# Kernel tuning notes

Hardware: AMD Instinct MI355X
Metric: run time of the kernel (lower is better)

## Reference

```python
import jax, jax.numpy as jnp
import numpy as np

BIN_SIZE = 128
DIST_MULT = 0.1
LN_EPS = 1e-6


def setup_inputs() -> dict:
    key = jax.random.key(0)
    ks = jax.random.split(key, 24)
    B, N, D, DD, H = 8, 25600, 256, 128, 128
    s = 0.02
    inp = {
        'x': jax.random.normal(ks[0], (B, N, D), dtype=jnp.float32),
        'msk': jax.random.randint(ks[1], (B, N), 0, 2) > 0,
        'ln_g': jnp.ones((D,), jnp.float32),
        'ln_b': jnp.zeros((D,), jnp.float32),
        # ffn_dist: Linear(256,128) ELU Linear(128,128) ELU Linear(128,128)
        'w1': s * jax.random.normal(ks[2], (D, H), jnp.float32),
        'b1': jnp.zeros((H,), jnp.float32),
        'w2': s * jax.random.normal(ks[3], (H, H), jnp.float32),
        'b2': jnp.zeros((H,), jnp.float32),
        'w3': s * jax.random.normal(ks[4], (H, DD), jnp.float32),
        'b3': jnp.zeros((DD,), jnp.float32),
        # LSH codebook random rotations [distance_dim, max_num_bins//2]
        'codebook': jax.random.normal(ks[5], (DD, 100), jnp.float32),
        # two GHConvDense layers, hidden_dim=output_dim=256
        'theta0': jax.random.normal(ks[6], (D, D), jnp.float32) * s,
        'wh0': jax.random.normal(ks[7], (D, D), jnp.float32) * s,
        'wt0': jax.random.normal(ks[8], (D, D), jnp.float32) * s,
        'bt0': jnp.zeros((D,), jnp.float32),
        'theta1': jax.random.normal(ks[9], (D, D), jnp.float32) * s,
        'wh1': jax.random.normal(ks[10], (D, D), jnp.float32) * s,
        'wt1': jax.random.normal(ks[11], (D, D), jnp.float32) * s,
        'bt1': jnp.zeros((D,), jnp.float32),
    }
    return inp


def _forward(x, msk, ln_g, ln_b, w1, b1, w2, b2, w3, b3, codebook,
             theta0, wh0, wt0, bt0, theta1, wh1, wt1, bt1):
    B, n_elems, D = x.shape
    pad = (-n_elems) % BIN_SIZE  # static python int
    if pad:
        x = jnp.pad(x, ((0, 0), (0, pad), (0, 0)))
        msk = jnp.pad(msk, ((0, 0), (0, pad)), constant_values=True)
    Np = n_elems + pad
    n_bins = Np // BIN_SIZE

    # layernorm
    mu = jnp.mean(x, -1, keepdims=True)
    var = jnp.mean(jnp.square(x - mu), -1, keepdims=True)
    xn = (x - mu) * jax.lax.rsqrt(var + LN_EPS) * ln_g + ln_b

    # distance FFN + dist activation (elu)
    h = jax.nn.elu(xn @ w1 + b1)
    h = jax.nn.elu(h @ w2 + b2)
    x_dist = jax.nn.elu(h @ w3 + b3)  # [B, Np, distance_dim]

    # LSH binning
    mul = x_dist @ codebook[:, :max(1, n_bins // 2)]
    cmul = jnp.concatenate([mul, -mul], axis=-1)  # [B, Np, n_bins]
    a = jnp.argmax(cmul, axis=-1)
    bin_idx = a + jnp.where(msk, 0, n_bins - 1)
    bins_split = jnp.argsort(bin_idx, axis=-1)  # [B, Np]

    # gather into bins
    xm = jnp.take_along_axis(x_dist, bins_split[..., None], axis=1)
    xm = xm.reshape(B, n_bins, BIN_SIZE, x_dist.shape[-1])
    xb = jnp.take_along_axis(xn, bins_split[..., None], axis=1)
    xb = xb.reshape(B, n_bins, BIN_SIZE, D)
    mskf = jnp.take_along_axis(msk, bins_split, axis=1)
    mskf = mskf.reshape(B, n_bins, BIN_SIZE, 1).astype(x.dtype)

    # pairwise Gaussian kernel within each bin
    xk = xm * mskf
    nsq = jnp.sum(jnp.square(xk), -1)  # [B, nb, P]
    inner = jnp.einsum('bnpd,bnqd->bnpq', xk, xk)
    d2 = nsq[..., :, None] - 2.0 * inner + nsq[..., None, :]
    dist = jnp.sqrt(jnp.clip(d2, 1e-6, 1e6))
    dm = jnp.clip(jnp.exp(-DIST_MULT * dist), 0.0, 1.0)
    dm = dm * mskf * jnp.swapaxes(mskf, -1, -2)  # mask rows & cols [B,nb,P,P]

    # gated graph convolutions
    for th, wh, wt, bt in ((theta0, wh0, wt0, bt0), (theta1, wh1, wt1, bt1)):
        xmk = xb * mskf
        f_hom = jnp.einsum('bnpq,bnqd->bnpd', dm, (xmk @ th) * mskf)
        f_het = xmk @ wh
        gate = jax.nn.sigmoid(xb @ wt + bt)
        xb = jax.nn.elu(gate * f_hom + (1.0 - gate) * f_het) * mskf

    # reverse LSH scatter
    xb_flat = xb.reshape(B, Np, D)
    ret = jax.vmap(lambda idx, pts: jnp.zeros((Np, D), pts.dtype).at[idx].set(pts))(
        bins_split, xb_flat)
    return ret[:, :n_elems, :]


def reference(x, msk, ln_g, ln_b, w1, b1, w2, b2, w3, b3, codebook,
              theta0, wh0, wt0, bt0, theta1, wh1, wt1, bt1):
    return _forward(x, msk, ln_g, ln_b, w1, b1, w2, b2, w3, b3, codebook,
                    theta0, wh0, wt0, bt0, theta1, wh1, wt1, bt1)
```

## Files before the change

kernel.cpp:

```cpp
#include <hip/hip_runtime.h>
#include <math.h>

#define B_ 8
#define NP_ 25600
#define T_ (B_*NP_)
#define D_ 256
#define H_ 128
#define DD_ 128
#define NBINS_ 200
#define NIDS_ 400
#define PB_ 128
#define NC_ 100
#define GT_ (B_*NBINS_)

typedef __attribute__((ext_vector_type(8))) short bf16x8;
typedef __attribute__((ext_vector_type(4))) float f32x4;
typedef __attribute__((ext_vector_type(4))) unsigned short u16x4;
typedef unsigned short u16;

__device__ __forceinline__ float eluf(float v){ return v > 0.f ? v : expm1f(v); }
__device__ __forceinline__ u16 f2bf(float f){
  union { float f; unsigned u; } v; v.f = f;
  unsigned r = v.u + 0x7fffu + ((v.u >> 16) & 1u);
  return (u16)(r >> 16);
}
__device__ __forceinline__ float bf2f(u16 h){
  union { unsigned u; float f; } v; v.u = ((unsigned)h) << 16; return v.f;
}

__device__ __forceinline__ void gl16(void* lds, const void* g){
  __builtin_amdgcn_global_load_lds((const __attribute__((address_space(1))) void*)g,
                                   (__attribute__((address_space(3))) void*)lds, 16, 0, 0);
}

__global__ void k_mask_detect(const unsigned int* __restrict__ m, int* __restrict__ flags){
  int any_f1 = 0, any_o = 0;
  for (int i = blockIdx.x*blockDim.x + threadIdx.x; i < T_/4; i += gridDim.x*blockDim.x){
    unsigned int w = m[i];
    if (w == 0x3F800000u) any_f1 = 1;
    else if (w > 1u) any_o = 1;
  }
  if (any_f1) atomicOr(&flags[0], 1);
  if (any_o)  atomicOr(&flags[1], 1);
}

__global__ void k_mask_convert(const void* __restrict__ m, const int* __restrict__ flags,
                               float* __restrict__ mskf){
  int i = blockIdx.x*256 + threadIdx.x;
  int mode = flags[0] ? 2 : (flags[1] ? 1 : 0);
  bool v;
  if (mode == 2)      v = ((const float*)m)[i] != 0.f;
  else if (mode == 1) v = ((const unsigned char*)m)[i] != 0;
  else                v = ((const int*)m)[i] != 0;
  mskf[i] = v ? 1.f : 0.f;
}

__global__ __launch_bounds__(256) void k_ln(const float* __restrict__ x,
    const float* __restrict__ g, const float* __restrict__ b, float* __restrict__ xn){
  const int wave = threadIdx.x >> 6, lane = threadIdx.x & 63;
  const long t = (long)blockIdx.x*4 + wave;
  float4 v = ((const float4*)(x + t*D_))[lane];
  float s  = v.x + v.y + v.z + v.w;
  float s2 = v.x*v.x + v.y*v.y + v.z*v.z + v.w*v.w;
  #pragma unroll
  for (int o = 32; o; o >>= 1){ s += __shfl_xor(s, o); s2 += __shfl_xor(s2, o); }
  const float mu = s * (1.f/D_);
  float var = s2*(1.f/D_) - mu*mu;
  var = fmaxf(var, 0.f);
  const float rs = rsqrtf(var + 1e-6f);
  float4 gg = ((const float4*)g)[lane];
  float4 bb = ((const float4*)b)[lane];
  float4 o4;
  o4.x = (v.x-mu)*rs*gg.x + bb.x;
  o4.y = (v.y-mu)*rs*gg.y + bb.y;
  o4.z = (v.z-mu)*rs*gg.z + bb.z;
  o4.w = (v.w-mu)*rs*gg.w + bb.w;
  ((float4*)(xn + t*D_))[lane] = o4;
}

template<int K>
__global__ __launch_bounds__(256) void k_gemm2(const float* __restrict__ A,
    const float* __restrict__ W, const float* __restrict__ bias, float* __restrict__ C){
  __shared__ __align__(16) float As[32*132];
  __shared__ __align__(16) float Bs[32*132];
  const size_t m0 = (size_t)blockIdx.x * 128;
  const int tid = threadIdx.x;
  const int tm = tid >> 4, tn = tid & 15;
  float acc[8][8] = {};
  for (int kc = 0; kc < K; kc += 32){
    __syncthreads();
    {
      const int r = tid >> 1, kq = (tid & 1) * 16;
      const float* src = &A[(m0 + r)*(size_t)K + kc + kq];
      #pragma unroll
      for (int q = 0; q < 4; ++q){
        const float4 v = ((const float4*)src)[q];
        As[(kq + q*4 + 0)*132 + r] = v.x;
        As[(kq + q*4 + 1)*132 + r] = v.y;
        As[(kq + q*4 + 2)*132 + r] = v.z;
        As[(kq + q*4 + 3)*132 + r] = v.w;
      }
      const int kk = tid >> 3, n0 = (tid & 7) * 16;
      const float* wsrc = &W[(size_t)(kc + kk)*128 + n0];
      #pragma unroll
      for (int q = 0; q < 4; ++q)
        *(float4*)&Bs[kk*132 + n0 + q*4] = ((const float4*)wsrc)[q];
    }
    __syncthreads();
    #pragma unroll
    for (int k = 0; k < 32; ++k){
      float a[8], b[8];
      *(float4*)&a[0] = *(const float4*)&As[k*132 + tm*4];
      *(float4*)&a[4] = *(const float4*)&As[k*132 + 64 + tm*4];
      *(float4*)&b[0] = *(const float4*)&Bs[k*132 + tn*4];
      *(float4*)&b[4] = *(const float4*)&Bs[k*132 + 64 + tn*4];
      #pragma unroll
      for (int i = 0; i < 8; ++i)
        #pragma unroll
        for (int j = 0; j < 8; ++j)
          acc[i][j] = fmaf(a[i], b[j], acc[i][j]);
    }
  }
  #pragma unroll
  for (int i = 0; i < 8; ++i){
    const size_t row = m0 + (i < 4 ? tm*4 + i : 64 + tm*4 + (i-4));
    #pragma unroll
    for (int q = 0; q < 2; ++q){
      const int c0 = q ? 64 + tn*4 : tn*4;
      float4 o;
      o.x = eluf(acc[i][q*4+0] + bias[c0+0]);
      o.y = eluf(acc[i][q*4+1] + bias[c0+1]);
      o.z = eluf(acc[i][q*4+2] + bias[c0+2]);
      o.w = eluf(acc[i][q*4+3] + bias[c0+3]);
      *(float4*)&C[row*128 + c0] = o;
    }
  }
}

__global__ void k_cbpad(const float* __restrict__ cb, float* __restrict__ cbp){
  const int k = blockIdx.x, c = threadIdx.x;
  cbp[k*128 + c] = (c < NC_) ? cb[k*NC_ + c] : 0.f;
}

__global__ __launch_bounds__(256) void k_mulmax(const float* __restrict__ A,
    const float* __restrict__ CB, const float* __restrict__ mskf, int* __restrict__ bidx){
  __shared__ __align__(16) float As[32*132];
  __shared__ __align__(16) float Bs[32*132];
  const size_t m0 = (size_t)blockIdx.x * 128;
  const int tid = threadIdx.x;
  const int tm = tid >> 4, tn = tid & 15;
  float acc[8][8] = {};
  for (int kc = 0; kc < DD_; kc += 32){
    __syncthreads();
    {
      const int r = tid >> 1, kq = (tid & 1) * 16;
      const float* src = &A[(m0 + r)*(size_t)DD_ + kc + kq];
      #pragma unroll
      for (int q = 0; q < 4; ++q){
        const float4 v = ((const float4*)src)[q];
        As[(kq + q*4 + 0)*132 + r] = v.x;
        As[(kq + q*4 + 1)*132 + r] = v.y;
        As[(kq + q*4 + 2)*132 + r] = v.z;
        As[(kq + q*4 + 3)*132 + r] = v.w;
      }
      const int kk = tid >> 3, n0 = (tid & 7) * 16;
      const float* wsrc = &CB[(size_t)(kc + kk)*128 + n0];
      #pragma unroll
      for (int q = 0; q < 4; ++q)
        *(float4*)&Bs[kk*132 + n0 + q*4] = ((const float4*)wsrc)[q];
    }
    __syncthreads();
    #pragma unroll
    for (int k = 0; k < 32; ++k){
      float a[8], b[8];
      *(float4*)&a[0] = *(const float4*)&As[k*132 + tm*4];
      *(float4*)&a[4] = *(const float4*)&As[k*132 + 64 + tm*4];
      *(float4*)&b[0] = *(const float4*)&Bs[k*132 + tn*4];
      *(float4*)&b[4] = *(const float4*)&Bs[k*132 + 64 + tn*4];
      #pragma unroll
      for (int i = 0; i < 8; ++i)
        #pragma unroll
        for (int j = 0; j < 8; ++j)
          acc[i][j] = fmaf(a[i], b[j], acc[i][j]);
    }
  }
  #pragma unroll
  for (int i = 0; i < 8; ++i){
    float bv = -1e30f; int bi = 0;
    #pragma unroll
    for (int j = 0; j < 8; ++j){
      const int c = (j < 4 ? tn*4 + j : 64 + tn*4 + (j-4));
      if (c < NC_){
        const float v = acc[i][j];
        if (v > bv || (v == bv && c < bi)){ bv = v; bi = c; }
        const float nv = -v; const int nc2 = c + NC_;
        if (nv > bv || (nv == bv && nc2 < bi)){ bv = nv; bi = nc2; }
      }
    }
    #pragma unroll
    for (int o = 1; o < 16; o <<= 1){
      const float ov = __shfl_xor(bv, o);
      const int oi = __shfl_xor(bi, o);
      if (ov > bv || (ov == bv && oi < bi)){ bv = ov; bi = oi; }
    }
    if (tn == 0){
      const size_t t = m0 + (i < 4 ? tm*4 + i : 64 + tm*4 + (i-4));
      bidx[t] = bi + (mskf[t] != 0.f ? 0 : NBINS_ - 1);
    }
  }
}

__global__ void k_hist(const int* __restrict__ bidx, int* __restrict__ hist){
  const int i = blockIdx.x*256 + threadIdx.x;
  const int b = i / NP_;
  atomicAdd(&hist[b*NIDS_ + bidx[i]], 1);
}

__global__ void k_prefix(const int* __restrict__ hist, int* __restrict__ offs){
  const int b = threadIdx.x;
  if (b < B_){
    int run = 0;
    for (int v = 0; v < NIDS_; ++v){ offs[b*NIDS_ + v] = run; run += hist[b*NIDS_ + v]; }
  }
}

__global__ __launch_bounds__(64) void k_binsort(const int* __restrict__ bidx,
    const int* __restrict__ offs, const int* __restrict__ hist, int* __restrict__ split){
  const int bv = blockIdx.x;
  if (hist[bv] == 0) return;
  const int b = bv / NIDS_, v = bv % NIDS_;
  int base = offs[bv];
  const int lane = threadIdx.x;
  const int* row = bidx + b*NP_;
  for (int i0 = 0; i0 < NP_; i0 += 64){
    const int i = i0 + lane;
    const bool m = (row[i] == v);
    const unsigned long long mk = __ballot(m);
    if (m){
      const int pos = base + __popcll(mk & ((1ull << lane) - 1ull));
      split[b*NP_ + pos] = i;
    }
    base += __popcll(mk);
  }
}

__global__ __launch_bounds__(256) void k_gather(const float* __restrict__ xn,
    const float* __restrict__ xd, const float* __restrict__ mskf,
    const int* __restrict__ split, u16* __restrict__ xmh,
    u16* __restrict__ xkh, float* __restrict__ mskg){
  const long j = (long)blockIdx.x*4 + (threadIdx.x >> 6);
  const int lane = threadIdx.x & 63;
  const int b = (int)(j / NP_);
  const int i = split[j];
  const long src = (long)b*NP_ + i;
  const float mv = mskf[src];
  const float4 v = ((const float4*)(xn + src*D_))[lane];
  u16x4 o;
  o[0] = f2bf(v.x*mv); o[1] = f2bf(v.y*mv); o[2] = f2bf(v.z*mv); o[3] = f2bf(v.w*mv);
  ((u16x4*)(xmh + j*D_))[lane] = o;
  if (lane < 32){
    const float4 ww = ((const float4*)(xd + src*DD_))[lane];
    u16x4 ow;
    ow[0] = f2bf(ww.x*mv); ow[1] = f2bf(ww.y*mv); ow[2] = f2bf(ww.z*mv); ow[3] = f2bf(ww.w*mv);
    ((u16x4*)(xkh + j*DD_))[lane] = ow;
  }
  if (lane == 0) mskg[j] = mv;
}

__global__ __launch_bounds__(256) void k_wt(const float* __restrict__ W, u16* __restrict__ o){
  const int n = blockIdx.x, k = threadIdx.x;
  o[n*D_ + k] = f2bf(W[k*D_ + n]);
}
__global__ __launch_bounds__(256) void k_wt2(const float* __restrict__ wt,
    const float* __restrict__ wh, u16* __restrict__ o){
  const int n = blockIdx.x, k = threadIdx.x;
  const float v = (n < 256) ? wt[(size_t)k*D_ + n] : wh[(size_t)k*D_ + (n-256)];
  o[(size_t)n*D_ + k] = f2bf(v);
}

__device__ __forceinline__ void stage64a(const u16* __restrict__ g, size_t row0,
    int ld, int k0, u16* Ls, int tid){
  const int w = tid >> 6, l = tid & 63;
  #pragma unroll
  for (int s = 0; s < 4; ++s){
    const int G = (s*4 + w)*64 + l;
    const int r = G >> 3, c8 = G & 7;
    gl16(&Ls[G*8], &g[(row0 + r)*(size_t)ld + k0 + ((c8 ^ (r & 7))*8)]);
  }
}
__device__ __forceinline__ void stage128a(const u16* __restrict__ g, size_t row0,
    int ld, u16* Ls, int tid){
  const int w = tid >> 6, l = tid & 63;
  #pragma unroll
  for (int s = 0; s < 8; ++s){
    const int G = (s*4 + w)*64 + l;
    const int r = G >> 4, c8 = G & 15;
    gl16(&Ls[G*8], &g[(row0 + r)*(size_t)ld + ((c8 ^ (r & 7))*8)]);
  }
}
__device__ __forceinline__ bf16x8 ldf(const u16* Ls, int row, int c8, int ldc8){
  return *(const bf16x8*)&Ls[(row*ldc8 + (c8 ^ (row & 7)))*8];
}

__global__ __launch_bounds__(256) void k_dm(const u16* __restrict__ xk,
    const float* __restrict__ rm, u16* __restrict__ dmb){
  __shared__ __align__(16) u16 Xs[128*128];
  __shared__ float nsq[128];
  __shared__ float msl[128];
  const int g = blockIdx.x;
  const int tid = threadIdx.x, l = tid & 63, wid = tid >> 6;
  const int wr = wid >> 1, wc = wid & 1, lm = l & 15, lk = l >> 4;
  stage128a(xk, (size_t)g*128, DD_, Xs, tid);
  if (tid < 128) msl[tid] = rm[(size_t)g*128 + tid];
  __syncthreads();
  f32x4 acc[4][4] = {};
  #pragma unroll
  for (int ks = 0; ks < 4; ++ks){
    bf16x8 a[4], b[4];
    #pragma unroll
    for (int mi = 0; mi < 4; ++mi) a[mi] = ldf(Xs, wr*64 + mi*16 + lm, ks*4 + lk, 16);
    #pragma unroll
    for (int ni = 0; ni < 4; ++ni) b[ni] = ldf(Xs, wc*64 + ni*16 + lm, ks*4 + lk, 16);
    #pragma unroll
    for (int mi = 0; mi < 4; ++mi)
      #pragma unroll
      for (int ni = 0; ni < 4; ++ni)
        acc[mi][ni] = __builtin_amdgcn_mfma_f32_16x16x32_bf16(a[mi], b[ni], acc[mi][ni], 0, 0, 0);
  }
  if (wr == wc && ((lm >> 2) == lk)){
    #pragma unroll
    for (int mi = 0; mi < 4; ++mi)
      nsq[wr*64 + mi*16 + lm] = acc[mi][mi][lm & 3];
  }
  __syncthreads();
  #pragma unroll
  for (int mi = 0; mi < 4; ++mi)
    #pragma unroll
    for (int ni = 0; ni < 4; ++ni)
      #pragma unroll
      for (int r = 0; r < 4; ++r){
        const int row = wr*64 + mi*16 + lk*4 + r;
        const int col = wc*64 + ni*16 + lm;
        float d2 = nsq[row] + nsq[col] - 2.f*acc[mi][ni][r];
        d2 = fminf(fmaxf(d2, 1e-6f), 1e6f);
        float w = expf(-0.1f * sqrtf(d2));
        w = fminf(w, 1.f);
        dmb[((size_t)g*PB_ + row)*PB_ + col] = f2bf(w * msl[row] * msl[col]);
      }
}

template<int OUT>
__global__ __launch_bounds__(256, 2) void k_fuse(const u16* __restrict__ dmb,
    const u16* __restrict__ thT, const u16* __restrict__ wtwh,
    const u16* __restrict__ X, const float* __restrict__ btv,
    const int* __restrict__ split, u16* __restrict__ o16, float* __restrict__ o32){
  __shared__ __align__(16) u16 bufA[128*128];
  __shared__ __align__(16) u16 bufB[128*128];
  __shared__ int ssp[128];
  const int h = blockIdx.x, g = blockIdx.y;
  const int tid = threadIdx.x, l = tid & 63, wid = tid >> 6;
  const int wr = wid >> 1, wc = wid & 1, lm = l & 15, lk = l >> 4;
  u16* SBw = bufB;
  u16* SBh = bufB + 128*64;
  if (OUT){ if (tid < 128) ssp[tid] = split[g*128 + tid]; }
  f32x4 at[4][4] = {}, ah[4][4] = {};
  for (int kt = 0; kt < 4; ++kt){
    __syncthreads();
    stage64a(X,    (size_t)g*128,       D_, kt*64, bufA, tid);
    stage64a(wtwh, (size_t)h*128,       D_, kt*64, SBw, tid);
    stage64a(wtwh, (size_t)(256+h*128), D_, kt*64, SBh, tid);
    __syncthreads();
    #pragma unroll
    for (int ks = 0; ks < 2; ++ks){
      bf16x8 xa[4], bt_[4], bh_[4];
      #pragma unroll
      for (int mi = 0; mi < 4; ++mi) xa[mi] = ldf(bufA, wr*64 + mi*16 + lm, ks*4 + lk, 8);
      #pragma unroll
      for (int ni = 0; ni < 4; ++ni){
        bt_[ni] = ldf(SBw, wc*64 + ni*16 + lm, ks*4 + lk, 8);
        bh_[ni] = ldf(SBh, wc*64 + ni*16 + lm, ks*4 + lk, 8);
      }
      #pragma unroll
      for (int mi = 0; mi < 4; ++mi)
        #pragma unroll
        for (int ni = 0; ni < 4; ++ni){
          at[mi][ni] = __builtin_amdgcn_mfma_f32_16x16x32_bf16(xa[mi], bt_[ni], at[mi][ni], 0, 0, 0);
          ah[mi][ni] = __builtin_amdgcn_mfma_f32_16x16x32_bf16(xa[mi], bh_[ni], ah[mi][ni], 0, 0, 0);
        }
    }
  }
  u16x4 atp[4][4], ahp[4][4];
  #pragma unroll
  for (int mi = 0; mi < 4; ++mi)
    #pragma unroll
    for (int ni = 0; ni < 4; ++ni)
      #pragma unroll
      for (int r = 0; r < 4; ++r){
        atp[mi][ni][r] = f2bf(at[mi][ni][r]);
        ahp[mi][ni][r] = f2bf(ah[mi][ni][r]);
      }
  f32x4 a1[4][4] = {};
  for (int kt = 0; kt < 4; ++kt){
    __syncthreads();
    stage64a(thT, (size_t)h*128, D_, kt*64, bufA, tid);
    stage64a(X,   (size_t)g*128, D_, kt*64, bufB, tid);
    __syncthreads();
    #pragma unroll
    for (int ks = 0; ks < 2; ++ks){
      bf16x8 a[4], b[4];
      #pragma unroll
      for (int mi = 0; mi < 4; ++mi) a[mi] = ldf(bufA, wr*64 + mi*16 + lm, ks*4 + lk, 8);
      #pragma unroll
      for (int ni = 0; ni < 4; ++ni) b[ni] = ldf(bufB, wc*64 + ni*16 + lm, ks*4 + lk, 8);
      #pragma unroll
      for (int mi = 0; mi < 4; ++mi)
        #pragma unroll
        for (int ni = 0; ni < 4; ++ni)
          a1[mi][ni] = __builtin_amdgcn_mfma_f32_16x16x32_bf16(a[mi], b[ni], a1[mi][ni], 0, 0, 0);
    }
  }
  __syncthreads();
  #pragma unroll
  for (int mi = 0; mi < 4; ++mi)
    #pragma unroll
    for (int ni = 0; ni < 4; ++ni)
      #pragma unroll
      for (int r = 0; r < 4; ++r){
        const int row = wr*64 + mi*16 + lk*4 + r;
        const int col = wc*64 + ni*16 + lm;
        bufB[(row*16 + ((col >> 3) ^ (row & 7)))*8 + (col & 7)] = f2bf(a1[mi][ni][r]);
      }
  stage128a(dmb, (size_t)g*128, PB_, bufA, tid);
  __syncthreads();
  f32x4 acc[4][4] = {};
  #pragma unroll
  for (int ks = 0; ks < 4; ++ks){
    bf16x8 a[4], b[4];
    #pragma unroll
    for (int mi = 0; mi < 4; ++mi) a[mi] = ldf(bufA, wr*64 + mi*16 + lm, ks*4 + lk, 16);
    #pragma unroll
    for (int ni = 0; ni < 4; ++ni) b[ni] = ldf(bufB, wc*64 + ni*16 + lm, ks*4 + lk, 16);
    #pragma unroll
    for (int mi = 0; mi < 4; ++mi)
      #pragma unroll
      for (int ni = 0; ni < 4; ++ni)
        acc[mi][ni] = __builtin_amdgcn_mfma_f32_16x16x32_bf16(a[mi], b[ni], acc[mi][ni], 0, 0, 0);
  }
  #pragma unroll
  for (int mi = 0; mi < 4; ++mi)
    #pragma unroll
    for (int ni = 0; ni < 4; ++ni){
      const int colc = wc*64 + ni*16 + lm;
      const int gc = h*128 + colc;
      const float bb = btv[gc];
      #pragma unroll
      for (int r = 0; r < 4; ++r){
        const int row = wr*64 + mi*16 + lk*4 + r;
        const float atv = bf2f(atp[mi][ni][r]);
        const float ahv = bf2f(ahp[mi][ni][r]);
        const float gt = 1.f/(1.f + expf(-(atv + bb)));
        const float o = eluf(gt*acc[mi][ni][r] + (1.f - gt)*ahv);
        if (OUT == 0){
          o16[((size_t)g*128 + row)*D_ + gc] = f2bf(o);
        } else {
          const int b = g / NBINS_;
          o32[((size_t)b*NP_ + ssp[row])*D_ + gc] = o;
        }
      }
    }
}

extern "C" void kernel_launch(void* const* d_in, const int* in_sizes, int n_in,
                              void* d_out, int out_size, void* d_ws, size_t ws_size,
                              hipStream_t stream){
  (void)in_sizes; (void)n_in; (void)out_size;
  const float* x    = (const float*)d_in[0];
  const void*  msk  = d_in[1];
  const float* ln_g = (const float*)d_in[2];
  const float* ln_b = (const float*)d_in[3];
  const float* w1 = (const float*)d_in[4];
  const float* b1 = (const float*)d_in[5];
  const float* w2 = (const float*)d_in[6];
  const float* b2 = (const float*)d_in[7];
  const float* w3 = (const float*)d_in[8];
  const float* b3 = (const float*)d_in[9];
  const float* cb = (const float*)d_in[10];
  const float* th0 = (const float*)d_in[11];
  const float* wh0 = (const float*)d_in[12];
  const float* wt0 = (const float*)d_in[13];
  const float* bt0 = (const float*)d_in[14];
  const float* th1 = (const float*)d_in[15];
  const float* wh1 = (const float*)d_in[16];
  const float* wt1 = (const float*)d_in[17];
  const float* bt1 = (const float*)d_in[18];
  float* out = (float*)d_out;

  char* ws = (char*)d_ws;
  size_t off = 0;
  auto alloc = [&](size_t bytes) -> void* {
    void* p = ws + off; off += (bytes + 255) & ~(size_t)255; return p;
  };
  int* flags = (int*)alloc(2*sizeof(int));
  int* hist  = (int*)alloc((size_t)B_*NIDS_*4);
  int* offs  = (int*)alloc((size_t)B_*NIDS_*4);
  int* bidx  = (int*)alloc((size_t)T_*4);
  int* split = (int*)alloc((size_t)T_*4);
  float* mskf = (float*)alloc((size_t)T_*4);
  float* mskg = (float*)alloc((size_t)T_*4);
  float* cbp = (float*)alloc((size_t)128*128*4);
  u16* thT0 = (u16*)alloc((size_t)D_*D_*2);
  u16* thT1 = (u16*)alloc((size_t)D_*D_*2);
  u16* wtwh0 = (u16*)alloc((size_t)512*D_*2);
  u16* wtwh1 = (u16*)alloc((size_t)512*D_*2);
  char* regA = (char*)alloc((size_t)T_*512*2);
  u16* xmh = (u16*)alloc((size_t)T_*D_*2);
  char* regC = (char*)alloc((size_t)T_*D_*2);
  u16* xb1 = (u16*)alloc((size_t)T_*D_*2);
  if (off > ws_size) return;

  float* P = (float*)regA;
  float* Q = P + (size_t)T_*DD_;
  u16* xkh = (u16*)regC;
  u16* dmb = xkh + (size_t)T_*DD_;
  float* xn = out;

  hipMemsetAsync(flags, 0, 2*sizeof(int), stream);
  hipMemsetAsync(hist, 0, (size_t)B_*NIDS_*4, stream);

  k_mask_detect<<<64, 256, 0, stream>>>((const unsigned int*)msk, flags);
  k_mask_convert<<<T_/256, 256, 0, stream>>>(msk, flags, mskf);

  k_ln<<<T_/4, 256, 0, stream>>>(x, ln_g, ln_b, xn);

  k_cbpad<<<128, 128, 0, stream>>>(cb, cbp);
  k_wt<<<256, 256, 0, stream>>>(th0, thT0);
  k_wt<<<256, 256, 0, stream>>>(th1, thT1);
  k_wt2<<<512, 256, 0, stream>>>(wt0, wh0, wtwh0);
  k_wt2<<<512, 256, 0, stream>>>(wt1, wh1, wtwh1);

  k_gemm2<D_><<<T_/128, 256, 0, stream>>>(xn, w1, b1, P);
  k_gemm2<H_><<<T_/128, 256, 0, stream>>>(P, w2, b2, Q);
  k_gemm2<H_><<<T_/128, 256, 0, stream>>>(Q, w3, b3, P);

  k_mulmax<<<T_/128, 256, 0, stream>>>(P, cbp, mskf, bidx);
  k_hist<<<T_/256, 256, 0, stream>>>(bidx, hist);
  k_prefix<<<1, 64, 0, stream>>>(hist, offs);
  k_binsort<<<B_*NIDS_, 64, 0, stream>>>(bidx, offs, hist, split);

  k_gather<<<T_/4, 256, 0, stream>>>(xn, P, mskf, split, xmh, xkh, mskg);
  k_dm<<<GT_, 256, 0, stream>>>(xkh, mskg, dmb);

  k_fuse<0><<<dim3(2, GT_), 256, 0, stream>>>(dmb, thT0, wtwh0, xmh, bt0, nullptr, xb1, nullptr);
  k_fuse<1><<<dim3(2, GT_), 256, 0, stream>>>(dmb, thT1, wtwh1, xb1, bt1, split, nullptr, out);
}
```

Before: 1.295 ms.

## Merge GEMM passes in fused graph-conv kernel, remap blocks, coalesce output stores

The theta GEMM is merged into the gate/het GEMM loop, so the X tile is staged once per k-step and reused for all three products instead of being reloaded in a second pass. Blocks are launched on a 1D grid and remapped with an XCD-style swizzle so neighbouring groups share cache locality. Epilogue results go to shared memory first and are then written with 16-byte vector stores, including the scattered fp32 output rows. This keeps a third accumulator set live, raising register pressure, and adds an extra barrier.

```diff
diff --git a/kernel.cpp b/kernel.cpp
--- a/kernel.cpp
+++ b/kernel.cpp
@@ -354,39 +354,59 @@
     const u16* __restrict__ thT, const u16* __restrict__ wtwh,
     const u16* __restrict__ X, const float* __restrict__ btv,
     const int* __restrict__ split, u16* __restrict__ o16, float* __restrict__ o32){
-  __shared__ __align__(16) u16 bufA[128*128];
-  __shared__ __align__(16) u16 bufB[128*128];
+  __shared__ __align__(16) u16 smem[32768];
   __shared__ int ssp[128];
-  const int h = blockIdx.x, g = blockIdx.y;
+  u16* bufA = smem;
+  u16* bufB = smem + 16384;
+  const int bid = blockIdx.x;
+  const int id = (bid & 7)*400 + (bid >> 3);
+  const int h = id & 1, g = id >> 1;
   const int tid = threadIdx.x, l = tid & 63, wid = tid >> 6;
   const int wr = wid >> 1, wc = wid & 1, lm = l & 15, lk = l >> 4;
-  u16* SBw = bufB;
-  u16* SBh = bufB + 128*64;
+  u16* stX = bufA;
+  u16* stT = bufA + 8192;
+  u16* stW = bufB;
+  u16* stH = bufB + 8192;
   if (OUT){ if (tid < 128) ssp[tid] = split[g*128 + tid]; }
-  f32x4 at[4][4] = {}, ah[4][4] = {};
+  f32x4 at[4][4] = {}, ah[4][4] = {}, a1[4][4] = {};
   for (int kt = 0; kt < 4; ++kt){
     __syncthreads();
-    stage64a(X,    (size_t)g*128,       D_, kt*64, bufA, tid);
-    stage64a(wtwh, (size_t)h*128,       D_, kt*64, SBw, tid);
-    stage64a(wtwh, (size_t)(256+h*128), D_, kt*64, SBh, tid);
+    stage64a(X,    (size_t)g*128,       D_, kt*64, stX, tid);
+    stage64a(thT,  (size_t)h*128,       D_, kt*64, stT, tid);
+    stage64a(wtwh, (size_t)h*128,       D_, kt*64, stW, tid);
+    stage64a(wtwh, (size_t)(256+h*128), D_, kt*64, stH, tid);
     __syncthreads();
     #pragma unroll
     for (int ks = 0; ks < 2; ++ks){
-      bf16x8 xa[4], bt_[4], bh_[4];
-      #pragma unroll
-      for (int mi = 0; mi < 4; ++mi) xa[mi] = ldf(bufA, wr*64 + mi*16 + lm, ks*4 + lk, 8);
-      #pragma unroll
-      for (int ni = 0; ni < 4; ++ni){
-        bt_[ni] = ldf(SBw, wc*64 + ni*16 + lm, ks*4 + lk, 8);
-        bh_[ni] = ldf(SBh, wc*64 + ni*16 + lm, ks*4 + lk, 8);
-      }
-      #pragma unroll
-      for (int mi = 0; mi < 4; ++mi)
+      {
+        bf16x8 ta[4], xb[4];
+        #pragma unroll
+        for (int mi = 0; mi < 4; ++mi) ta[mi] = ldf(stT, wr*64 + mi*16 + lm, ks*4 + lk, 8);
+        #pragma unroll
+        for (int ni = 0; ni < 4; ++ni) xb[ni] = ldf(stX, wc*64 + ni*16 + lm, ks*4 + lk, 8);
+        #pragma unroll
+        for (int mi = 0; mi < 4; ++mi)
+          #pragma unroll
+          for (int ni = 0; ni < 4; ++ni)
+            a1[mi][ni] = __builtin_amdgcn_mfma_f32_16x16x32_bf16(ta[mi], xb[ni], a1[mi][ni], 0, 0, 0);
+      }
+      {
+        bf16x8 xa[4], wtf[4], whf[4];
+        #pragma unroll
+        for (int mi = 0; mi < 4; ++mi) xa[mi] = ldf(stX, wr*64 + mi*16 + lm, ks*4 + lk, 8);
         #pragma unroll
         for (int ni = 0; ni < 4; ++ni){
-          at[mi][ni] = __builtin_amdgcn_mfma_f32_16x16x32_bf16(xa[mi], bt_[ni], at[mi][ni], 0, 0, 0);
-          ah[mi][ni] = __builtin_amdgcn_mfma_f32_16x16x32_bf16(xa[mi], bh_[ni], ah[mi][ni], 0, 0, 0);
+          wtf[ni] = ldf(stW, wc*64 + ni*16 + lm, ks*4 + lk, 8);
+          whf[ni] = ldf(stH, wc*64 + ni*16 + lm, ks*4 + lk, 8);
         }
+        #pragma unroll
+        for (int mi = 0; mi < 4; ++mi)
+          #pragma unroll
+          for (int ni = 0; ni < 4; ++ni){
+            at[mi][ni] = __builtin_amdgcn_mfma_f32_16x16x32_bf16(xa[mi], wtf[ni], at[mi][ni], 0, 0, 0);
+            ah[mi][ni] = __builtin_amdgcn_mfma_f32_16x16x32_bf16(xa[mi], whf[ni], ah[mi][ni], 0, 0, 0);
+          }
+      }
     }
   }
   u16x4 atp[4][4], ahp[4][4];
@@ -399,26 +419,6 @@
         atp[mi][ni][r] = f2bf(at[mi][ni][r]);
         ahp[mi][ni][r] = f2bf(ah[mi][ni][r]);
       }
-  f32x4 a1[4][4] = {};
-  for (int kt = 0; kt < 4; ++kt){
-    __syncthreads();
-    stage64a(thT, (size_t)h*128, D_, kt*64, bufA, tid);
-    stage64a(X,   (size_t)g*128, D_, kt*64, bufB, tid);
-    __syncthreads();
-    #pragma unroll
-    for (int ks = 0; ks < 2; ++ks){
-      bf16x8 a[4], b[4];
-      #pragma unroll
-      for (int mi = 0; mi < 4; ++mi) a[mi] = ldf(bufA, wr*64 + mi*16 + lm, ks*4 + lk, 8);
-      #pragma unroll
-      for (int ni = 0; ni < 4; ++ni) b[ni] = ldf(bufB, wc*64 + ni*16 + lm, ks*4 + lk, 8);
-      #pragma unroll
-      for (int mi = 0; mi < 4; ++mi)
-        #pragma unroll
-        for (int ni = 0; ni < 4; ++ni)
-          a1[mi][ni] = __builtin_amdgcn_mfma_f32_16x16x32_bf16(a[mi], b[ni], a1[mi][ni], 0, 0, 0);
-    }
-  }
   __syncthreads();
   #pragma unroll
   for (int mi = 0; mi < 4; ++mi)
@@ -446,28 +446,54 @@
       for (int ni = 0; ni < 4; ++ni)
         acc[mi][ni] = __builtin_amdgcn_mfma_f32_16x16x32_bf16(a[mi], b[ni], acc[mi][ni], 0, 0, 0);
   }
-  #pragma unroll
-  for (int mi = 0; mi < 4; ++mi)
-    #pragma unroll
-    for (int ni = 0; ni < 4; ++ni){
-      const int colc = wc*64 + ni*16 + lm;
-      const int gc = h*128 + colc;
-      const float bb = btv[gc];
-      #pragma unroll
-      for (int r = 0; r < 4; ++r){
-        const int row = wr*64 + mi*16 + lk*4 + r;
-        const float atv = bf2f(atp[mi][ni][r]);
-        const float ahv = bf2f(ahp[mi][ni][r]);
-        const float gt = 1.f/(1.f + expf(-(atv + bb)));
-        const float o = eluf(gt*acc[mi][ni][r] + (1.f - gt)*ahv);
-        if (OUT == 0){
-          o16[((size_t)g*128 + row)*D_ + gc] = f2bf(o);
-        } else {
-          const int b = g / NBINS_;
-          o32[((size_t)b*NP_ + ssp[row])*D_ + gc] = o;
+  __syncthreads();
+  if (OUT == 0){
+    #pragma unroll
+    for (int mi = 0; mi < 4; ++mi)
+      #pragma unroll
+      for (int ni = 0; ni < 4; ++ni){
+        const int colc = wc*64 + ni*16 + lm;
+        const float bb = btv[h*128 + colc];
+        #pragma unroll
+        for (int r = 0; r < 4; ++r){
+          const int row = wr*64 + mi*16 + lk*4 + r;
+          const float gt = 1.f/(1.f + expf(-(bf2f(atp[mi][ni][r]) + bb)));
+          const float o = eluf(gt*acc[mi][ni][r] + (1.f - gt)*bf2f(ahp[mi][ni][r]));
+          bufA[row*128 + colc] = f2bf(o);
         }
       }
-    }
+    __syncthreads();
+    #pragma unroll
+    for (int s = 0; s < 8; ++s){
+      const int G = s*256 + tid;
+      const int r = G >> 4, c8 = G & 15;
+      *(bf16x8*)&o16[((size_t)g*128 + r)*D_ + h*128 + c8*8] = *(const bf16x8*)&bufA[r*128 + c8*8];
+    }
+  } else {
+    float* fb = (float*)smem;
+    #pragma unroll
+    for (int mi = 0; mi < 4; ++mi)
+      #pragma unroll
+      for (int ni = 0; ni < 4; ++ni){
+        const int colc = wc*64 + ni*16 + lm;
+        const float bb = btv[h*128 + colc];
+        #pragma unroll
+        for (int r = 0; r < 4; ++r){
+          const int row = wr*64 + mi*16 + lk*4 + r;
+          const float gt = 1.f/(1.f + expf(-(bf2f(atp[mi][ni][r]) + bb)));
+          fb[row*128 + colc] = eluf(gt*acc[mi][ni][r] + (1.f - gt)*bf2f(ahp[mi][ni][r]));
+        }
+      }
+    __syncthreads();
+    const int b = g / NBINS_;
+    #pragma unroll
+    for (int s = 0; s < 16; ++s){
+      const int G = s*256 + tid;
+      const int r = G >> 5, c4 = G & 31;
+      const float4 v = *(const float4*)&fb[r*128 + c4*4];
+      *(float4*)&o32[((size_t)b*NP_ + ssp[r])*D_ + h*128 + c4*4] = v;
+    }
+  }
 }
 
 extern "C" void kernel_launch(void* const* d_in, const int* in_sizes, int n_in,
@@ -550,6 +576,6 @@
   k_gather<<<T_/4, 256, 0, stream>>>(xn, P, mskf, split, xmh, xkh, mskg);
   k_dm<<<GT_, 256, 0, stream>>>(xkh, mskg, dmb);
 
-  k_fuse<0><<<dim3(2, GT_), 256, 0, stream>>>(dmb, thT0, wtwh0, xmh, bt0, nullptr, xb1, nullptr);
-  k_fuse<1><<<dim3(2, GT_), 256, 0, stream>>>(dmb, thT1, wtwh1, xb1, bt1, split, nullptr, out);
-}
+  k_fuse<0><<<2*GT_, 256, 0, stream>>>(dmb, thT0, wtwh0, xmh, bt0, nullptr, xb1, nullptr);
+  k_fuse<1><<<2*GT_, 256, 0, stream>>>(dmb, thT1, wtwh1, xb1, bt1, split, nullptr, out);
+}
```

Measured after the change: 1.455 ms. +12.4%, slower.
